# Optimization experiments

Measured on AMD Instinct MI355X. Metric: run time of the kernel, lower is better.

Reference implementation:

```python
import jax, jax.numpy as jnp
import numpy as np

N, H, P, L, E, F = 131072, 256, 32768, 16, 8, 16
FUSED = 3 * H + E + F  # 792


def setup_inputs() -> dict:
    key = jax.random.key(0)
    ks = jax.random.split(key, 8)
    return {
        "node_embs": jax.random.normal(ks[0], (N, H), jnp.float32),
        "path_nodes": jax.random.randint(ks[1], (P, L), 0, N),
        "path_lens": jax.random.randint(ks[2], (P,), 0, L + 1),
        "path_edge_feats": jax.random.normal(ks[3], (P, E), jnp.float32),
        "path_scalar_feats": jax.random.normal(ks[4], (P, F), jnp.float32),
        "W1": jax.random.normal(ks[5], (FUSED, H), jnp.float32) / np.float32(np.sqrt(FUSED)),
        "b1": jnp.zeros((H,), jnp.float32),
        "W2": jax.random.normal(ks[6], (H, 1), jnp.float32) / np.float32(np.sqrt(H)),
        "b2": jnp.zeros((1,), jnp.float32),
        "src_idx": 0,
        "dst_idx": 1,
    }


def reference(node_embs, path_nodes, path_lens, path_edge_feats, path_scalar_feats,
              W1, b1, W2, b2, src_idx, dst_idx):
    dt = node_embs.dtype
    # ragged per-path mean over node embeddings, padded to [P, L]
    mask = (jnp.arange(L)[None, :] < path_lens[:, None]).astype(dt)  # [P, L]
    gathered = node_embs[path_nodes]                                  # [P, L, H]
    denom = jnp.maximum(path_lens, 1).astype(dt)[:, None]             # [P, 1]
    path_emb = jnp.einsum('plh,pl->ph', gathered, mask) / denom       # [P, H]

    src = jnp.broadcast_to(node_embs[src_idx], (P, H))
    dst = jnp.broadcast_to(node_embs[dst_idx], (P, H))
    fused = jnp.concatenate([src, dst, path_emb, path_edge_feats, path_scalar_feats], axis=1)  # [P, FUSED]

    h = jax.nn.relu(fused @ W1 + b1)   # [P, H]
    q = (h @ W2 + b2)[:, 0]            # [P]
    # empty paths produce exactly 0.0, matching the torch branch
    return jnp.where(path_lens > 0, q, jnp.zeros((), dt))
```

## Files before the change

kernel.cpp:

```cpp
#include <hip/hip_runtime.h>

#define NN      131072
#define H       256
#define PPATHS  32768
#define LMAX    16
#define EF      8
#define FF      16
#define KP      288
#define TPB     16
#define FS      296

typedef short v8s __attribute__((ext_vector_type(8)));
typedef float v4f __attribute__((ext_vector_type(4)));

__device__ __forceinline__ unsigned short f2bf(float x) {
    unsigned int u = __float_as_uint(x);
    u += 0x7fffu + ((u >> 16) & 1u);
    return (unsigned short)(u >> 16);
}

__global__ __launch_bounds__(256) void prep_kernel(
        const float* __restrict__ node_embs,
        const float* __restrict__ W1,
        const float* __restrict__ b1,
        const int*   __restrict__ si,
        const int*   __restrict__ di,
        unsigned short* __restrict__ W1T,
        float*       __restrict__ cvec) {
    __shared__ float red[256];
    const int b = blockIdx.x;
    if (b < KP) {
        const int k = b, n = threadIdx.x;
        float v = 0.0f;
        if (k < 256)      v = W1[(size_t)(512 + k) * H + n];
        else if (k < 280) v = W1[(size_t)(768 + (k - 256)) * H + n];
        W1T[(size_t)n * KP + k] = f2bf(v);
    } else {
        const int jb = b - KP;
        const int t  = threadIdx.x;
        const int jl = t & 3, kp = t >> 2;
        const int j  = jb * 4 + jl;
        const float* src = node_embs + (size_t)si[0] * H;
        const float* dst = node_embs + (size_t)di[0] * H;
        float c = 0.0f;
        #pragma unroll
        for (int i = 0; i < 8; ++i) {
            int k = kp + i * 64;
            float f = (k < H) ? src[k] : dst[k - H];
            c += f * W1[(size_t)k * H + j];
        }
        red[t] = c;
        __syncthreads();
        for (int s = 128; s >= 4; s >>= 1) {
            if (t < s) red[t] += red[t + s];
            __syncthreads();
        }
        if (t < 4) cvec[jb * 4 + t] = b1[jb * 4 + t] + red[t];
    }
}

__global__ __launch_bounds__(256, 6) void fused_kernel(
        const float* __restrict__ node_embs,
        const int*   __restrict__ path_nodes,
        const int*   __restrict__ path_lens,
        const float* __restrict__ edge_f,
        const float* __restrict__ scal_f,
        const unsigned short* __restrict__ W1T,
        const float* __restrict__ cvec,
        const float* __restrict__ W2,
        const float* __restrict__ b2,
        float*       __restrict__ out) {
    __shared__ __align__(16) unsigned short feat[TPB * FS];
    __shared__ float qpart[TPB][5];

    const int tid  = threadIdx.x;
    const int wave = tid >> 6, lane = tid & 63;
    const int pb   = blockIdx.x * TPB;

    for (int i = tid; i < TPB * 32; i += 256) {
        const int p = i >> 5, s = i & 31;
        float v = 0.0f;
        if (s < EF)           v = edge_f[(size_t)(pb + p) * EF + s];
        else if (s < EF + FF) v = scal_f[(size_t)(pb + p) * FF + (s - EF)];
        feat[p * FS + H + s] = f2bf(v);
    }

    for (int pi = 0; pi < 4; ++pi) {
        const int p   = wave * 4 + pi;
        const int gp  = pb + p;
        const int len = path_lens[gp];
        const int iv  = path_nodes[(size_t)gp * LMAX + (lane & 15)];

        float4 a0 = make_float4(0, 0, 0, 0), a1 = make_float4(0, 0, 0, 0);
        float4 a2 = make_float4(0, 0, 0, 0), a3 = make_float4(0, 0, 0, 0);
        int l = 0;
        for (; l + 3 < len; l += 4) {
            const int n0 = __shfl(iv, l);
            const int n1 = __shfl(iv, l + 1);
            const int n2 = __shfl(iv, l + 2);
            const int n3 = __shfl(iv, l + 3);
            const float4 v0 = ((const float4*)(node_embs + (size_t)n0 * H))[lane];
            const float4 v1 = ((const float4*)(node_embs + (size_t)n1 * H))[lane];
            const float4 v2 = ((const float4*)(node_embs + (size_t)n2 * H))[lane];
            const float4 v3 = ((const float4*)(node_embs + (size_t)n3 * H))[lane];
            a0.x += v0.x; a0.y += v0.y; a0.z += v0.z; a0.w += v0.w;
            a1.x += v1.x; a1.y += v1.y; a1.z += v1.z; a1.w += v1.w;
            a2.x += v2.x; a2.y += v2.y; a2.z += v2.z; a2.w += v2.w;
            a3.x += v3.x; a3.y += v3.y; a3.z += v3.z; a3.w += v3.w;
        }
        for (; l < len; ++l) {
            const int n0 = __shfl(iv, l);
            const float4 v0 = ((const float4*)(node_embs + (size_t)n0 * H))[lane];
            a0.x += v0.x; a0.y += v0.y; a0.z += v0.z; a0.w += v0.w;
        }
        const float inv = 1.0f / (float)max(len, 1);
        ushort4 r;
        r.x = f2bf((a0.x + a1.x + a2.x + a3.x) * inv);
        r.y = f2bf((a0.y + a1.y + a2.y + a3.y) * inv);
        r.z = f2bf((a0.z + a1.z + a2.z + a3.z) * inv);
        r.w = f2bf((a0.w + a1.w + a2.w + a3.w) * inv);
        *(ushort4*)&feat[p * FS + 4 * lane] = r;
    }
    __syncthreads();

    const int col = lane & 15, quad = lane >> 4;
    const int n0  = wave * 64;

    v4f acc[4];
    float w2v[4];
    #pragma unroll
    for (int nt = 0; nt < 4; ++nt) {
        const float cv = cvec[n0 + nt * 16 + col];
        w2v[nt] = W2[n0 + nt * 16 + col];
        acc[nt] = (v4f){cv, cv, cv, cv};
    }

    const unsigned short* Alds  = feat + col * FS + quad * 8;
    const unsigned short* Bbase = W1T + (size_t)(n0 + col) * KP + quad * 8;

    for (int k0 = 0; k0 < KP; k0 += 32) {
        v8s a, b[4];
        a = *(const v8s*)(Alds + k0);
        #pragma unroll
        for (int nt = 0; nt < 4; ++nt)
            b[nt] = *(const v8s*)(Bbase + (size_t)(nt * 16) * KP + k0);
        #pragma unroll
        for (int nt = 0; nt < 4; ++nt)
            acc[nt] = __builtin_amdgcn_mfma_f32_16x16x32_bf16(
                          a, b[nt], acc[nt], 0, 0, 0);
    }

    {
        float s[4];
        #pragma unroll
        for (int r = 0; r < 4; ++r) {
            float v = 0.0f;
            #pragma unroll
            for (int nt = 0; nt < 4; ++nt)
                v += fmaxf(acc[nt][r], 0.0f) * w2v[nt];
            s[r] = v;
        }
        #pragma unroll
        for (int off = 1; off < 16; off <<= 1) {
            #pragma unroll
            for (int r = 0; r < 4; ++r)
                s[r] += __shfl_xor(s[r], off);
        }
        if (col == 0) {
            #pragma unroll
            for (int r = 0; r < 4; ++r)
                qpart[quad * 4 + r][wave] = s[r];
        }
    }
    __syncthreads();

    if (tid < TPB) {
        const float q = qpart[tid][0] + qpart[tid][1] + qpart[tid][2] + qpart[tid][3] + b2[0];
        out[pb + tid] = (path_lens[pb + tid] > 0) ? q : 0.0f;
    }
}

extern "C" void kernel_launch(void* const* d_in, const int* in_sizes, int n_in,
                              void* d_out, int out_size, void* d_ws, size_t ws_size,
                              hipStream_t stream) {
    const float* node_embs  = (const float*)d_in[0];
    const int*   path_nodes = (const int*)d_in[1];
    const int*   path_lens  = (const int*)d_in[2];
    const float* edge_f     = (const float*)d_in[3];
    const float* scal_f     = (const float*)d_in[4];
    const float* W1         = (const float*)d_in[5];
    const float* b1         = (const float*)d_in[6];
    const float* W2         = (const float*)d_in[7];
    const float* b2         = (const float*)d_in[8];
    const int*   si         = (const int*)d_in[9];
    const int*   di         = (const int*)d_in[10];
    float* out = (float*)d_out;

    float*          cvec = (float*)d_ws;
    unsigned short* W1T  = (unsigned short*)((char*)d_ws + 1024);

    hipLaunchKernelGGL(prep_kernel, dim3(KP + 64), dim3(256), 0, stream,
                       node_embs, W1, b1, si, di, W1T, cvec);
    hipLaunchKernelGGL(fused_kernel, dim3(PPATHS / TPB), dim3(256), 0, stream,
                       node_embs, path_nodes, path_lens, edge_f, scal_f,
                       W1T, cvec, W2, b2, out);
}
```

Before: 238.0 us.

## Pre-convert node embeddings to bf16 and gather half-width rows in 8-deep batches

Adds a pass that converts the whole node embedding table to bf16 in workspace. The fused kernel then gathers bf16 rows instead of fp32, halving the bytes per gathered row. The gather loop is also restructured to issue up to 8 independent row loads per chunk, using readlane for node indices and a uniform path length. In exchange, every call pays a full read of the fp32 table plus a bf16 write, and the node values are rounded to bf16 before they are averaged. The new path runs only when the workspace is large enough, and falls back to the fp32 gather otherwise.

Measured after the change: 251.5 us. +5.7%, slower.

```diff
diff --git a/kernel.cpp b/kernel.cpp
--- a/kernel.cpp
+++ b/kernel.cpp
@@ -12,11 +12,26 @@
 
 typedef short v8s __attribute__((ext_vector_type(8)));
 typedef float v4f __attribute__((ext_vector_type(4)));
+typedef unsigned short v8u __attribute__((ext_vector_type(8)));
 
 __device__ __forceinline__ unsigned short f2bf(float x) {
     unsigned int u = __float_as_uint(x);
     u += 0x7fffu + ((u >> 16) & 1u);
     return (unsigned short)(u >> 16);
+}
+__device__ __forceinline__ float bf2f(unsigned short u) {
+    return __uint_as_float((unsigned int)u << 16);
+}
+
+__global__ __launch_bounds__(256) void cvt_kernel(
+        const float* __restrict__ ne, unsigned short* __restrict__ t) {
+    const size_t i = ((size_t)blockIdx.x * 256 + threadIdx.x) * 8;
+    const v4f a = __builtin_nontemporal_load((const v4f*)(ne + i));
+    const v4f b = __builtin_nontemporal_load((const v4f*)(ne + i + 4));
+    v8u r;
+    r[0] = f2bf(a.x); r[1] = f2bf(a.y); r[2] = f2bf(a.z); r[3] = f2bf(a.w);
+    r[4] = f2bf(b.x); r[5] = f2bf(b.y); r[6] = f2bf(b.z); r[7] = f2bf(b.w);
+    *(v8u*)(t + i) = r;
 }
 
 __global__ __launch_bounds__(256) void prep_kernel(
@@ -59,8 +74,10 @@
     }
 }
 
+template<bool B16>
 __global__ __launch_bounds__(256, 6) void fused_kernel(
         const float* __restrict__ node_embs,
+        const unsigned short* __restrict__ ne16,
         const int*   __restrict__ path_nodes,
         const int*   __restrict__ path_lens,
         const float* __restrict__ edge_f,
@@ -88,37 +105,46 @@
     for (int pi = 0; pi < 4; ++pi) {
         const int p   = wave * 4 + pi;
         const int gp  = pb + p;
-        const int len = path_lens[gp];
+        const int len = __builtin_amdgcn_readfirstlane(path_lens[gp]);
         const int iv  = path_nodes[(size_t)gp * LMAX + (lane & 15)];
 
-        float4 a0 = make_float4(0, 0, 0, 0), a1 = make_float4(0, 0, 0, 0);
-        float4 a2 = make_float4(0, 0, 0, 0), a3 = make_float4(0, 0, 0, 0);
-        int l = 0;
-        for (; l + 3 < len; l += 4) {
-            const int n0 = __shfl(iv, l);
-            const int n1 = __shfl(iv, l + 1);
-            const int n2 = __shfl(iv, l + 2);
-            const int n3 = __shfl(iv, l + 3);
-            const float4 v0 = ((const float4*)(node_embs + (size_t)n0 * H))[lane];
-            const float4 v1 = ((const float4*)(node_embs + (size_t)n1 * H))[lane];
-            const float4 v2 = ((const float4*)(node_embs + (size_t)n2 * H))[lane];
-            const float4 v3 = ((const float4*)(node_embs + (size_t)n3 * H))[lane];
-            a0.x += v0.x; a0.y += v0.y; a0.z += v0.z; a0.w += v0.w;
-            a1.x += v1.x; a1.y += v1.y; a1.z += v1.z; a1.w += v1.w;
-            a2.x += v2.x; a2.y += v2.y; a2.z += v2.z; a2.w += v2.w;
-            a3.x += v3.x; a3.y += v3.y; a3.z += v3.z; a3.w += v3.w;
-        }
-        for (; l < len; ++l) {
-            const int n0 = __shfl(iv, l);
-            const float4 v0 = ((const float4*)(node_embs + (size_t)n0 * H))[lane];
-            a0.x += v0.x; a0.y += v0.y; a0.z += v0.z; a0.w += v0.w;
+        v4f a = {0.0f, 0.0f, 0.0f, 0.0f};
+        #pragma unroll
+        for (int c = 0; c < 2; ++c) {
+            const int base = c * 8;
+            ushort4 vb[8];
+            float4  vf[8];
+            if (base < len) {
+                #pragma unroll
+                for (int l = 0; l < 8; ++l) {
+                    if (base + l < len) {
+                        const int n = __builtin_amdgcn_readlane(iv, base + l);
+                        if constexpr (B16)
+                            vb[l] = ((const ushort4*)(ne16 + (size_t)n * H))[lane];
+                        else
+                            vf[l] = ((const float4*)(node_embs + (size_t)n * H))[lane];
+                    }
+                }
+                #pragma unroll
+                for (int l = 0; l < 8; ++l) {
+                    if (base + l < len) {
+                        if constexpr (B16) {
+                            a.x += bf2f(vb[l].x); a.y += bf2f(vb[l].y);
+                            a.z += bf2f(vb[l].z); a.w += bf2f(vb[l].w);
+                        } else {
+                            a.x += vf[l].x; a.y += vf[l].y;
+                            a.z += vf[l].z; a.w += vf[l].w;
+                        }
+                    }
+                }
+            }
         }
         const float inv = 1.0f / (float)max(len, 1);
         ushort4 r;
-        r.x = f2bf((a0.x + a1.x + a2.x + a3.x) * inv);
-        r.y = f2bf((a0.y + a1.y + a2.y + a3.y) * inv);
-        r.z = f2bf((a0.z + a1.z + a2.z + a3.z) * inv);
-        r.w = f2bf((a0.w + a1.w + a2.w + a3.w) * inv);
+        r.x = f2bf(a.x * inv);
+        r.y = f2bf(a.y * inv);
+        r.z = f2bf(a.z * inv);
+        r.w = f2bf(a.w * inv);
         *(ushort4*)&feat[p * FS + 4 * lane] = r;
     }
     __syncthreads();
@@ -198,10 +224,21 @@
 
     float*          cvec = (float*)d_ws;
     unsigned short* W1T  = (unsigned short*)((char*)d_ws + 1024);
-
+    unsigned short* NE16 = (unsigned short*)((char*)d_ws + 262144);
+    const size_t need = 262144 + (size_t)NN * H * 2;
+    const bool big = ws_size >= need;
+
+    if (big)
+        hipLaunchKernelGGL(cvt_kernel, dim3((NN * H) / (256 * 8)), dim3(256), 0, stream,
+                           node_embs, NE16);
     hipLaunchKernelGGL(prep_kernel, dim3(KP + 64), dim3(256), 0, stream,
                        node_embs, W1, b1, si, di, W1T, cvec);
-    hipLaunchKernelGGL(fused_kernel, dim3(PPATHS / TPB), dim3(256), 0, stream,
-                       node_embs, path_nodes, path_lens, edge_f, scal_f,
-                       W1T, cvec, W2, b2, out);
-}
+    if (big)
+        hipLaunchKernelGGL(fused_kernel<true>, dim3(PPATHS / TPB), dim3(256), 0, stream,
+                           node_embs, NE16, path_nodes, path_lens, edge_f, scal_f,
+                           W1T, cvec, W2, b2, out);
+    else
+        hipLaunchKernelGGL(fused_kernel<false>, dim3(PPATHS / TPB), dim3(256), 0, stream,
+                           node_embs, NE16, path_nodes, path_lens, edge_f, scal_f,
+                           W1T, cvec, W2, b2, out);
+}
```
